# Optimization experiments

Measured on AMD Instinct MI355X. Metric: run time of the kernel, lower is better.

Reference implementation:

```python
import jax, jax.numpy as jnp
import numpy as np

C = 1.0          # ball curvature (c in MidpointMLR)
B = 1048576      # batch
F_IN = 64        # num_features
F_OUT = 64       # num_classes
EPS = 1e-15


def setup_inputs() -> dict:
    key = jax.random.key(0)
    k1, k2, k3 = jax.random.split(key, 3)
    # points well inside the Poincare ball
    x = 0.05 * jax.random.normal(k1, (B, F_IN), dtype=jnp.float32)
    # PoincareLinear params: z [in, out], bias [out]
    z = jax.random.normal(k2, (F_IN, F_OUT), dtype=jnp.float32) * (1.0 / np.sqrt(F_IN))
    bias = 0.01 * jax.random.normal(k3, (F_OUT,), dtype=jnp.float32)
    return {"x": x, "z": z, "bias": bias}


def reference(x, z, bias):
    """HNN++ PoincareLinear: unidirectional Poincare MLR + map back into the ball."""
    c = jnp.float32(C)
    rc = jnp.sqrt(c)
    # split z into direction and magnitude (column-wise)
    z_norm = jnp.maximum(jnp.linalg.norm(z, axis=0), EPS)   # [out]
    z_unit = z / z_norm                                      # [in, out]
    # unidirectional Poincare MLR logits
    rcx = rc * x                                             # [B, in]
    cx2 = jnp.sum(rcx * rcx, axis=-1, keepdims=True)         # [B, 1] = c*||x||^2
    drcr = 2.0 * rc * bias                                   # [out]
    num = 2.0 * (rcx @ z_unit) * jnp.cosh(drcr) - (1.0 + cx2) * jnp.sinh(drcr)
    logits = (2.0 * z_norm / rc) * jnp.arcsinh(num / jnp.maximum(1.0 - cx2, EPS))  # [B, out]
    # map distances back onto the ball: x -> sinh(rc*x)/rc, then gyro-projection
    y = jnp.sinh(rc * logits) / rc
    return y / (1.0 + jnp.sqrt(1.0 + c * jnp.sum(y * y, axis=-1, keepdims=True)))
```

## Files before the change

kernel.cpp:

```cpp
#include <hip/hip_runtime.h>
#include <math.h>


#define MLR_B 1048576

typedef __bf16 bf16x8 __attribute__((ext_vector_type(8)));
typedef float  f32x4  __attribute__((ext_vector_type(4)));

__global__ __launch_bounds__(256) void mlr_prep_kernel(const float* __restrict__ z,
                                                       const float* __restrict__ bias,
                                                       void* __restrict__ wsv) {
    __bf16* zf   = (__bf16*)wsv;
    f32x4*  cst4 = (f32x4*)((char*)wsv + 8192);
    __shared__ float part[4][64];
    __shared__ float invs[64];

    const int tid = threadIdx.x;
    const int o   = tid & 63;
    const int kq  = tid >> 6;

    float n2 = 0.f;
#pragma unroll
    for (int kk = 0; kk < 16; ++kk) {
        int k = kq * 16 + kk;
        float v = z[k * 64 + o];
        n2 = fmaf(v, v, n2);
    }
    part[kq][o] = n2;
    __syncthreads();

    if (tid < 64) {
        float tot = part[0][o] + part[1][o] + part[2][o] + part[3][o];
        float zn  = fmaxf(sqrtf(tot), 1e-15f);
        invs[o] = 1.f / zn;
        float d = 2.f * bias[o];
        cst4[o] = (f32x4){2.f * coshf(d), sinhf(d), 2.f * zn, 0.f};
    }
    __syncthreads();

    const float inv = invs[o];
    const int t = o & 3, c = o >> 2;
#pragma unroll
    for (int kk = 0; kk < 16; ++kk) {
        int k  = kq * 16 + kk;
        float zu = z[k * 64 + o] * inv;
        int i  = k >> 4;
        int j  = k & 3;
        int hi = (k >> 2) & 3;
        int s  = i >> 1;
        int e  = ((i & 1) << 2) | j;
        zf[(s * 4 + t) * 512 + (hi * 16 + c) * 8 + e] = (__bf16)zu;
    }
}

__device__ __forceinline__ float poin_y(float dot, float ch2, float sh, float g,
                                        float opc, float rden) {
    float t = fmaf(dot, ch2, -(opc * sh)) * rden;
    float u = t + sqrtf(fmaf(t, t, 1.f));
    float w = __builtin_amdgcn_exp2f(g * __builtin_amdgcn_logf(u));
    return 0.5f * (w - __builtin_amdgcn_rcpf(w));
}

struct StepMid {
    f32x4 acc[4];
    float p;
};

__device__ __forceinline__ StepMid mlr_gemm(f32x4 c0, f32x4 c1, f32x4 c2, f32x4 c3,
                                            const bf16x8* bfr) {
    StepMid m;
    float p = 0.f;
#pragma unroll
    for (int j = 0; j < 4; ++j) {
        p = fmaf(c0[j], c0[j], p); p = fmaf(c1[j], c1[j], p);
        p = fmaf(c2[j], c2[j], p); p = fmaf(c3[j], c3[j], p);
    }
    p += __shfl_xor(p, 16);
    p += __shfl_xor(p, 32);
    m.p = p;

    bf16x8 a0, a1;
#pragma unroll
    for (int j = 0; j < 4; ++j) {
        a0[j]     = (__bf16)c0[j];
        a0[4 + j] = (__bf16)c1[j];
        a1[j]     = (__bf16)c2[j];
        a1[4 + j] = (__bf16)c3[j];
    }

#pragma unroll
    for (int t = 0; t < 4; ++t) {
        m.acc[t] = (f32x4){0.f, 0.f, 0.f, 0.f};
        m.acc[t] = __builtin_amdgcn_mfma_f32_16x16x32_bf16(a0, bfr[t],     m.acc[t], 0, 0, 0);
        m.acc[t] = __builtin_amdgcn_mfma_f32_16x16x32_bf16(a1, bfr[4 + t], m.acc[t], 0, 0, 0);
    }
    return m;
}

__device__ __forceinline__ void mlr_fin(const StepMid& m, const f32x4* cc,
                                        int lo, int hi, char* ob) {
    f32x4 yv[4]; float S[4];
#pragma unroll
    for (int r = 0; r < 4; ++r) {
        float cxr  = __shfl(m.p, hi * 4 + r);
        float opc  = 1.f + cxr;
        float rden = __builtin_amdgcn_rcpf(fmaxf(1.f - cxr, 1e-15f));
        float s0 = 0.f;
        f32x4 y;
#pragma unroll
        for (int t = 0; t < 4; ++t) {
            float v = poin_y(m.acc[t][r], cc[t].x, cc[t].y, cc[t].z, opc, rden);
            y[t] = v;
            s0 = fmaf(v, v, s0);
        }
        yv[r] = y;
        S[r] = s0;
    }
#pragma unroll
    for (int r = 0; r < 4; ++r) {
        float s0 = S[r];
        s0 += __shfl_xor(s0, 1);
        s0 += __shfl_xor(s0, 2);
        s0 += __shfl_xor(s0, 4);
        s0 += __shfl_xor(s0, 8);
        float scale = __builtin_amdgcn_rcpf(1.f + sqrtf(1.f + s0));
        f32x4 y = yv[r];
        y[0] *= scale; y[1] *= scale; y[2] *= scale; y[3] *= scale;
        yv[r] = y;
    }
#pragma unroll
    for (int r = 0; r < 4; ++r)
        __builtin_nontemporal_store(yv[r], (f32x4*)(ob + r * 256));
}

__global__ __launch_bounds__(256, 4) void mlr_main_kernel(const float* __restrict__ x,
                                                          const void* __restrict__ wsv,
                                                          float* __restrict__ out) {
    const __bf16* zf   = (const __bf16*)wsv;
    const f32x4*  cst4 = (const f32x4*)((const char*)wsv + 8192);
    const int tid  = threadIdx.x;
    const int lane = tid & 63;
    const int lo   = lane & 15;
    const int hi   = lane >> 4;
    const int wv   = blockIdx.x * 4 + (tid >> 6);

    bf16x8 bfr[8];
#pragma unroll
    for (int i = 0; i < 8; ++i)
        bfr[i] = *(const bf16x8*)((const char*)zf + i * 1024 + lane * 16);
    f32x4 cc[4];
#pragma unroll
    for (int t = 0; t < 4; ++t) cc[t] = cst4[4 * lo + t];

    const size_t rowbase = (size_t)wv * 32;
    const char* xb = (const char*)x + (rowbase + (size_t)lo) * 256 + hi * 16;
    char* ob = (char*)out + (rowbase + (size_t)hi * 4) * 256 + lo * 16;

    f32x4 c0 = *(const f32x4*)(xb + 0);
    f32x4 c1 = *(const f32x4*)(xb + 64);
    f32x4 c2 = *(const f32x4*)(xb + 128);
    f32x4 c3 = *(const f32x4*)(xb + 192);

    StepMid m0 = mlr_gemm(c0, c1, c2, c3, bfr);

    f32x4 d0 = *(const f32x4*)(xb + 4096 + 0);
    f32x4 d1 = *(const f32x4*)(xb + 4096 + 64);
    f32x4 d2 = *(const f32x4*)(xb + 4096 + 128);
    f32x4 d3 = *(const f32x4*)(xb + 4096 + 192);

    mlr_fin(m0, cc, lo, hi, ob);

    StepMid m1 = mlr_gemm(d0, d1, d2, d3, bfr);
    mlr_fin(m1, cc, lo, hi, ob + 4096);
}

extern "C" void kernel_launch(void* const* d_in, const int* in_sizes, int n_in,
                              void* d_out, int out_size, void* d_ws, size_t ws_size,
                              hipStream_t stream) {
    const float* x    = (const float*)d_in[0];
    const float* z    = (const float*)d_in[1];
    const float* bias = (const float*)d_in[2];
    float* out = (float*)d_out;

    mlr_prep_kernel<<<dim3(1), dim3(256), 0, stream>>>(z, bias, d_ws);
    mlr_main_kernel<<<dim3(8192), dim3(256), 0, stream>>>(x, d_ws, out);
}
```

Baseline: 96.62 us.

## Stage x tiles through LDS with async global_load_lds and XOR swizzle

```diff
diff --git a/kernel.cpp b/kernel.cpp
--- a/kernel.cpp
+++ b/kernel.cpp
@@ -6,6 +6,11 @@
 
 typedef __bf16 bf16x8 __attribute__((ext_vector_type(8)));
 typedef float  f32x4  __attribute__((ext_vector_type(4)));
+
+#define GLOAD_LDS16(g, l)                                                              \
+    __builtin_amdgcn_global_load_lds(                                                  \
+        (const __attribute__((address_space(1))) void*)(g),                            \
+        (__attribute__((address_space(3))) void*)(l), 16, 0, 0)
 
 __global__ __launch_bounds__(256) void mlr_prep_kernel(const float* __restrict__ z,
                                                        const float* __restrict__ bias,
@@ -133,16 +138,31 @@
         __builtin_nontemporal_store(yv[r], (f32x4*)(ob + r * 256));
 }
 
-__global__ __launch_bounds__(256, 4) void mlr_main_kernel(const float* __restrict__ x,
-                                                          const void* __restrict__ wsv,
-                                                          float* __restrict__ out) {
+__global__ __launch_bounds__(256) void mlr_main_kernel(const float* __restrict__ x,
+                                                       const void* __restrict__ wsv,
+                                                       float* __restrict__ out) {
+    __shared__ char xs[32768];
     const __bf16* zf   = (const __bf16*)wsv;
     const f32x4*  cst4 = (const f32x4*)((const char*)wsv + 8192);
     const int tid  = threadIdx.x;
     const int lane = tid & 63;
     const int lo   = lane & 15;
     const int hi   = lane >> 4;
-    const int wv   = blockIdx.x * 4 + (tid >> 6);
+    const int w    = tid >> 6;
+    const int wv   = blockIdx.x * 4 + w;
+    const size_t rowbase = (size_t)wv * 32;
+
+    char* wbase = xs + w * 8192;
+    const char* xg = (const char*)x;
+
+#pragma unroll
+    for (int n = 0; n < 8; ++n) {
+        const int st = n >> 2, n2 = n & 3;
+        const int r  = n2 * 4 + hi;
+        const int ck = lo ^ r;
+        const char* src = xg + (rowbase + (size_t)(st * 16 + r)) * 256 + ck * 16;
+        GLOAD_LDS16(src, wbase + n * 1024);
+    }
 
     bf16x8 bfr[8];
 #pragma unroll
@@ -152,26 +172,21 @@
 #pragma unroll
     for (int t = 0; t < 4; ++t) cc[t] = cst4[4 * lo + t];
 
-    const size_t rowbase = (size_t)wv * 32;
-    const char* xb = (const char*)x + (rowbase + (size_t)lo) * 256 + hi * 16;
+    asm volatile("s_waitcnt vmcnt(0)" ::: "memory");
+    __builtin_amdgcn_sched_barrier(0);
+
     char* ob = (char*)out + (rowbase + (size_t)hi * 4) * 256 + lo * 16;
 
-    f32x4 c0 = *(const f32x4*)(xb + 0);
-    f32x4 c1 = *(const f32x4*)(xb + 64);
-    f32x4 c2 = *(const f32x4*)(xb + 128);
-    f32x4 c3 = *(const f32x4*)(xb + 192);
-
-    StepMid m0 = mlr_gemm(c0, c1, c2, c3, bfr);
-
-    f32x4 d0 = *(const f32x4*)(xb + 4096 + 0);
-    f32x4 d1 = *(const f32x4*)(xb + 4096 + 64);
-    f32x4 d2 = *(const f32x4*)(xb + 4096 + 128);
-    f32x4 d3 = *(const f32x4*)(xb + 4096 + 192);
-
-    mlr_fin(m0, cc, lo, hi, ob);
-
-    StepMid m1 = mlr_gemm(d0, d1, d2, d3, bfr);
-    mlr_fin(m1, cc, lo, hi, ob + 4096);
+#pragma unroll
+    for (int st = 0; st < 2; ++st) {
+        const char* sb = wbase + st * 4096 + lo * 256;
+        f32x4 c0 = *(const f32x4*)(sb + ((0  + hi) ^ lo) * 16);
+        f32x4 c1 = *(const f32x4*)(sb + ((4  + hi) ^ lo) * 16);
+        f32x4 c2 = *(const f32x4*)(sb + ((8  + hi) ^ lo) * 16);
+        f32x4 c3 = *(const f32x4*)(sb + ((12 + hi) ^ lo) * 16);
+        StepMid m = mlr_gemm(c0, c1, c2, c3, bfr);
+        mlr_fin(m, cc, lo, hi, ob + st * 4096);
+    }
 }
 
 extern "C" void kernel_launch(void* const* d_in, const int* in_sizes, int n_in,
```

After: 97.12 us. Within noise of the previous version (+0.5%).

## Fuse weight-prep kernel into main kernel, recomputing normalized z per block in LDS

Applied to the files above, without the earlier changes.

```diff
diff --git a/kernel.cpp b/kernel.cpp
--- a/kernel.cpp
+++ b/kernel.cpp
@@ -7,51 +7,7 @@
 typedef __bf16 bf16x8 __attribute__((ext_vector_type(8)));
 typedef float  f32x4  __attribute__((ext_vector_type(4)));
 
-__global__ __launch_bounds__(256) void mlr_prep_kernel(const float* __restrict__ z,
-                                                       const float* __restrict__ bias,
-                                                       void* __restrict__ wsv) {
-    __bf16* zf   = (__bf16*)wsv;
-    f32x4*  cst4 = (f32x4*)((char*)wsv + 8192);
-    __shared__ float part[4][64];
-    __shared__ float invs[64];
-
-    const int tid = threadIdx.x;
-    const int o   = tid & 63;
-    const int kq  = tid >> 6;
-
-    float n2 = 0.f;
-#pragma unroll
-    for (int kk = 0; kk < 16; ++kk) {
-        int k = kq * 16 + kk;
-        float v = z[k * 64 + o];
-        n2 = fmaf(v, v, n2);
-    }
-    part[kq][o] = n2;
-    __syncthreads();
-
-    if (tid < 64) {
-        float tot = part[0][o] + part[1][o] + part[2][o] + part[3][o];
-        float zn  = fmaxf(sqrtf(tot), 1e-15f);
-        invs[o] = 1.f / zn;
-        float d = 2.f * bias[o];
-        cst4[o] = (f32x4){2.f * coshf(d), sinhf(d), 2.f * zn, 0.f};
-    }
-    __syncthreads();
-
-    const float inv = invs[o];
-    const int t = o & 3, c = o >> 2;
-#pragma unroll
-    for (int kk = 0; kk < 16; ++kk) {
-        int k  = kq * 16 + kk;
-        float zu = z[k * 64 + o] * inv;
-        int i  = k >> 4;
-        int j  = k & 3;
-        int hi = (k >> 2) & 3;
-        int s  = i >> 1;
-        int e  = ((i & 1) << 2) | j;
-        zf[(s * 4 + t) * 512 + (hi * 16 + c) * 8 + e] = (__bf16)zu;
-    }
-}
+#define LOG2E 1.4426950408889634f
 
 __device__ __forceinline__ float poin_y(float dot, float ch2, float sh, float g,
                                         float opc, float rden) {
@@ -133,33 +89,82 @@
         __builtin_nontemporal_store(yv[r], (f32x4*)(ob + r * 256));
 }
 
-__global__ __launch_bounds__(256, 4) void mlr_main_kernel(const float* __restrict__ x,
-                                                          const void* __restrict__ wsv,
-                                                          float* __restrict__ out) {
-    const __bf16* zf   = (const __bf16*)wsv;
-    const f32x4*  cst4 = (const f32x4*)((const char*)wsv + 8192);
+__global__ __launch_bounds__(256, 4) void mlr_fused_kernel(const float* __restrict__ x,
+                                                           const float* __restrict__ z,
+                                                           const float* __restrict__ bias,
+                                                           float* __restrict__ out) {
+    __shared__ float  part[4][64];
+    __shared__ __bf16 zfl[4096];
+
     const int tid  = threadIdx.x;
     const int lane = tid & 63;
     const int lo   = lane & 15;
     const int hi   = lane >> 4;
-    const int wv   = blockIdx.x * 4 + (tid >> 6);
+    const int w    = tid >> 6;
+    const int o    = lane;
+    const int kq   = w;
+    const int wv   = blockIdx.x * 4 + w;
+    const size_t rowbase = (size_t)wv * 32;
+
+    float zv[16];
+#pragma unroll
+    for (int kk = 0; kk < 16; ++kk)
+        zv[kk] = z[(kq * 16 + kk) * 64 + o];
+
+    float bb[4];
+#pragma unroll
+    for (int t = 0; t < 4; ++t) bb[t] = bias[4 * lo + t];
+
+    const char* xb = (const char*)x + (rowbase + (size_t)lo) * 256 + hi * 16;
+    f32x4 c0 = *(const f32x4*)(xb + 0);
+    f32x4 c1 = *(const f32x4*)(xb + 64);
+    f32x4 c2 = *(const f32x4*)(xb + 128);
+    f32x4 c3 = *(const f32x4*)(xb + 192);
+
+    float n2 = 0.f;
+#pragma unroll
+    for (int kk = 0; kk < 16; ++kk) n2 = fmaf(zv[kk], zv[kk], n2);
+    part[kq][o] = n2;
+    asm volatile("s_waitcnt lgkmcnt(0)" ::: "memory");
+    __builtin_amdgcn_s_barrier();
+
+    float tot_own = part[0][o] + part[1][o] + part[2][o] + part[3][o];
+    float zn_own  = fmaxf(sqrtf(tot_own), 1e-15f);
+    float inv     = 1.f / zn_own;
+
+    f32x4 cc[4];
+#pragma unroll
+    for (int t = 0; t < 4; ++t) {
+        float tot_c = __shfl(tot_own, 4 * lo + t);
+        float zn_c  = fmaxf(sqrtf(tot_c), 1e-15f);
+        float e  = __builtin_amdgcn_exp2f(2.f * bb[t] * LOG2E);
+        float re = __builtin_amdgcn_rcpf(e);
+        cc[t] = (f32x4){e + re, 0.5f * (e - re), 2.f * zn_c, 0.f};
+    }
+
+    {
+        const int tf = o & 3, cs = o >> 2;
+#pragma unroll
+        for (int kk = 0; kk < 16; ++kk) {
+            int k  = kq * 16 + kk;
+            float zu = zv[kk] * inv;
+            int i  = k >> 4;
+            int j  = k & 3;
+            int h2 = (k >> 2) & 3;
+            int s  = i >> 1;
+            int e  = ((i & 1) << 2) | j;
+            zfl[(s * 4 + tf) * 512 + (h2 * 16 + cs) * 8 + e] = (__bf16)zu;
+        }
+    }
+    asm volatile("s_waitcnt lgkmcnt(0)" ::: "memory");
+    __builtin_amdgcn_s_barrier();
 
     bf16x8 bfr[8];
 #pragma unroll
     for (int i = 0; i < 8; ++i)
-        bfr[i] = *(const bf16x8*)((const char*)zf + i * 1024 + lane * 16);
-    f32x4 cc[4];
-#pragma unroll
-    for (int t = 0; t < 4; ++t) cc[t] = cst4[4 * lo + t];
+        bfr[i] = *(const bf16x8*)((const char*)zfl + i * 1024 + lane * 16);
 
-    const size_t rowbase = (size_t)wv * 32;
-    const char* xb = (const char*)x + (rowbase + (size_t)lo) * 256 + hi * 16;
     char* ob = (char*)out + (rowbase + (size_t)hi * 4) * 256 + lo * 16;
-
-    f32x4 c0 = *(const f32x4*)(xb + 0);
-    f32x4 c1 = *(const f32x4*)(xb + 64);
-    f32x4 c2 = *(const f32x4*)(xb + 128);
-    f32x4 c3 = *(const f32x4*)(xb + 192);
 
     StepMid m0 = mlr_gemm(c0, c1, c2, c3, bfr);
 
@@ -182,6 +187,5 @@
     const float* bias = (const float*)d_in[2];
     float* out = (float*)d_out;
 
-    mlr_prep_kernel<<<dim3(1), dim3(256), 0, stream>>>(z, bias, d_ws);
-    mlr_main_kernel<<<dim3(8192), dim3(256), 0, stream>>>(x, d_ws, out);
+    mlr_fused_kernel<<<dim3(8192), dim3(256), 0, stream>>>(x, z, bias, out);
 }
```

Result: no change. 95.58 us (-1.1%).
